# Kernel optimization log

Measured on AMD Instinct MI355X. Metric: run time of the kernel, lower is better.

The kernel has to match this reference:

```python
import jax, jax.numpy as jnp
import numpy as np

N = 8192
D_IN = 256
D_OUT = 256
DROP_P = 0.5


def setup_inputs() -> dict:
    key = jax.random.key(0)
    k1, k2, k3, k4, k5 = jax.random.split(key, 5)
    inputs = jax.random.normal(k1, (N, D_IN), dtype=jnp.float32)
    # torch nn.Linear weights are [d_out, d_in], applied as x @ W.T
    Wq = jax.random.normal(k2, (D_OUT, D_IN), dtype=jnp.float32) * (1.0 / np.sqrt(D_IN))
    Wk = jax.random.normal(k3, (D_OUT, D_IN), dtype=jnp.float32) * (1.0 / np.sqrt(D_IN))
    Wv = jax.random.normal(k4, (D_OUT, D_IN), dtype=jnp.float32) * (1.0 / np.sqrt(D_IN))
    # deterministic dropout keep-mask (True = keep), p=0.5
    drop_mask = jax.random.bernoulli(k5, 1.0 - DROP_P, (N, N))
    return {"inputs": inputs, "Wq": Wq, "Wk": Wk, "Wv": Wv, "drop_mask": drop_mask}


def reference(inputs, Wq, Wk, Wv, drop_mask):
    # QKV projections (no bias)
    q = inputs @ Wq.T  # [N, d_out]
    k = inputs @ Wk.T  # [N, d_out]
    v = inputs @ Wv.T  # [N, d_out]

    d_k = k.shape[1]
    scores = q @ k.T  # [N, N]

    # causal mask: strictly-upper-triangular entries -> -inf
    n = scores.shape[0]
    causal = jnp.triu(jnp.ones((n, n), dtype=bool), k=1)
    masked = jnp.where(causal, -jnp.inf, scores)

    attn_weights = jax.nn.softmax(masked / jnp.sqrt(jnp.float32(d_k)), axis=-1)

    # dropout p=0.5 in train mode: zero dropped entries, scale kept by 1/(1-p)
    scale = jnp.float32(1.0 / (1.0 - DROP_P))
    attn_weights = jnp.where(drop_mask, attn_weights * scale, 0.0)

    context_vector = attn_weights @ v  # [N, d_out]
    return context_vector
```

## Files before the change

### kernel.cpp

```cpp
#include <hip/hip_runtime.h>

#define NT 8192
#define DM 256

typedef float f32x16 __attribute__((ext_vector_type(16)));
typedef float f32x4 __attribute__((ext_vector_type(4)));
typedef __bf16 bf16x8 __attribute__((ext_vector_type(8)));
typedef unsigned int u32x4 __attribute__((ext_vector_type(4)));

#define MFMA32(a, b, c) __builtin_amdgcn_mfma_f32_32x32x16_bf16((a), (b), (c), 0, 0, 0)
#define MFMA16(a, b, c) __builtin_amdgcn_mfma_f32_16x16x32_bf16((a), (b), (c), 0, 0, 0)
#define NEG_INF (-__builtin_inff())

static __device__ __forceinline__ unsigned short f2bf_bits(float f) {
  return __builtin_bit_cast(unsigned short, (__bf16)f);
}
static __device__ __forceinline__ float exp2_fast(float x) {
  return __builtin_amdgcn_exp2f(x);
}
static __device__ __forceinline__ void gload_lds16(const void* g, void* l) {
  __builtin_amdgcn_global_load_lds(
      (const __attribute__((address_space(1))) unsigned int*)g,
      (__attribute__((address_space(3))) unsigned int*)l, 16, 0, 0);
}

__global__ __launch_bounds__(256) void maskpack_kernel(
    const void* __restrict__ mask, unsigned long long* __restrict__ bm) {
  const int t = threadIdx.x, lane = t & 63, w = t >> 6;
  const int r = blockIdx.x + (w << 11);
  const unsigned int* md = (const unsigned int*)mask;
  bool a01 = true, af = true;
#pragma unroll
  for (int k = 0; k < 4; ++k) {
    unsigned int v = md[lane + 64 * k];
    a01 = a01 && (v <= 1u);
    af = af && (v == 0u || v == 0x3F800000u);
  }
  const bool dword_mode = __all(a01) || __all(af);
  unsigned long long* out = bm + (size_t)r * 128;
  if (dword_mode) {
    const unsigned int* mk = (const unsigned int*)mask + (size_t)r * NT;
    const int iters = (r >> 8) + 1;
    for (int it = 0; it < iters; ++it) {
      const int j0 = it * 256;
      unsigned int v0 = mk[j0 + lane];
      unsigned int v1 = mk[j0 + 64 + lane];
      unsigned int v2 = mk[j0 + 128 + lane];
      unsigned int v3 = mk[j0 + 192 + lane];
      unsigned long long b0 = __ballot(v0 != 0u);
      unsigned long long b1 = __ballot(v1 != 0u);
      unsigned long long b2 = __ballot(v2 != 0u);
      unsigned long long b3 = __ballot(v3 != 0u);
      if (lane == 0) {
        out[(j0 >> 6) + 0] = b0;
        out[(j0 >> 6) + 1] = b1;
        out[(j0 >> 6) + 2] = b2;
        out[(j0 >> 6) + 3] = b3;
      }
    }
  } else {
    const unsigned char* mk = (const unsigned char*)mask + (size_t)r * NT;
    unsigned short* outs = (unsigned short*)out;
    const int iters = (r >> 10) + 1;
    for (int it = 0; it < iters; ++it) {
      const uint4 d = *(const uint4*)(mk + it * 1024 + lane * 16);
      unsigned int dws[4] = {d.x, d.y, d.z, d.w};
      unsigned int m16 = 0;
#pragma unroll
      for (int k = 0; k < 4; ++k) {
        unsigned int x = dws[k];
        x |= x >> 4;
        x |= x >> 2;
        x |= x >> 1;
        x &= 0x01010101u;
        m16 |= ((x * 0x01020408u) >> 24) << (4 * k);
      }
      outs[it * 64 + lane] = (unsigned short)m16;
    }
  }
}

__global__ __launch_bounds__(256) void proj_kernel(
    const float* __restrict__ X, const float* __restrict__ Wq,
    const float* __restrict__ Wk, const float* __restrict__ Wv,
    unsigned short* __restrict__ Qs, unsigned short* __restrict__ Kb,
    unsigned short* __restrict__ Vt) {
  __shared__ __align__(16) unsigned short Xs[64 * 256];
  __shared__ __align__(16) unsigned short Ws[64 * 256];
  __shared__ float Tr[4][32 * 33];
  const int ib = blockIdx.x, mat = blockIdx.y;
  const float* W = (mat == 0) ? Wq : (mat == 1) ? Wk : Wv;
  const float wscale = (mat == 0) ? 0.09016844005556021f : (mat == 2 ? 2.0f : 1.0f);
  const int t = threadIdx.x;
  const int lane = t & 63, w = t >> 6;
  const int m = lane & 31, half = lane >> 5;
  const int i0 = ib * 64;
#pragma unroll
  for (int cc = 0; cc < 8; ++cc) {
    int chunk = t + 256 * cc;
    int rr = chunk >> 5, c = chunk & 31;
    const float4* src = (const float4*)(X + (size_t)(i0 + rr) * 256 + c * 8);
    float4 f0 = src[0], f1 = src[1];
    bf16x8 v;
    v[0] = (__bf16)f0.x; v[1] = (__bf16)f0.y; v[2] = (__bf16)f0.z; v[3] = (__bf16)f0.w;
    v[4] = (__bf16)f1.x; v[5] = (__bf16)f1.y; v[6] = (__bf16)f1.z; v[7] = (__bf16)f1.w;
    *(bf16x8*)&Xs[(rr * 32 + (c ^ (rr & 31))) * 8] = v;
  }
  const int wr = w >> 1, wc = w & 1;
  for (int cb = 0; cb < 4; ++cb) {
    __syncthreads();
#pragma unroll
    for (int cc = 0; cc < 8; ++cc) {
      int chunk = t + 256 * cc;
      int rr = chunk >> 5, c = chunk & 31;
      const float4* src = (const float4*)(W + (size_t)(cb * 64 + rr) * 256 + c * 8);
      float4 f0 = src[0], f1 = src[1];
      bf16x8 v;
      v[0] = (__bf16)(f0.x * wscale); v[1] = (__bf16)(f0.y * wscale);
      v[2] = (__bf16)(f0.z * wscale); v[3] = (__bf16)(f0.w * wscale);
      v[4] = (__bf16)(f1.x * wscale); v[5] = (__bf16)(f1.y * wscale);
      v[6] = (__bf16)(f1.z * wscale); v[7] = (__bf16)(f1.w * wscale);
      *(bf16x8*)&Ws[(rr * 32 + (c ^ (rr & 31))) * 8] = v;
    }
    __syncthreads();
    f32x16 acc = {};
    const int ar = 32 * wr + m;
    const int br = 32 * wc + m;
#pragma unroll
    for (int st = 0; st < 16; ++st) {
      int kc = st * 2 + half;
      bf16x8 a = *(const bf16x8*)&Xs[(ar * 32 + (kc ^ (ar & 31))) * 8];
      bf16x8 b = *(const bf16x8*)&Ws[(br * 32 + (kc ^ (br & 31))) * 8];
      acc = MFMA32(a, b, acc);
    }
    if (mat < 2) {
      unsigned short* O = mat ? Kb : Qs;
#pragma unroll
      for (int r = 0; r < 16; ++r) {
        int row = i0 + 32 * wr + (r & 3) + 8 * (r >> 2) + 4 * half;
        int col = cb * 64 + 32 * wc + m;
        O[(size_t)row * DM + col] = f2bf_bits(acc[r]);
      }
    } else {
      float* T = Tr[w];
#pragma unroll
      for (int r = 0; r < 16; ++r) {
        int rl = (r & 3) + 8 * (r >> 2) + 4 * half;
        T[m * 33 + rl] = acc[r];
      }
      asm volatile("s_waitcnt lgkmcnt(0)" ::: "memory");
#pragma unroll
      for (int q = 0; q < 16; ++q) {
        int dl = 2 * q + half;
        float val = T[dl * 33 + m];
        Vt[(size_t)(cb * 64 + 32 * wc + dl) * NT + i0 + 32 * wr + m] = f2bf_bits(val);
      }
      asm volatile("s_waitcnt lgkmcnt(0)" ::: "memory");
    }
  }
}

__global__ __launch_bounds__(256, 3) void flash_kernel(
    const unsigned short* __restrict__ Qs, const unsigned short* __restrict__ Kg,
    const unsigned short* __restrict__ Vtg, const unsigned int* __restrict__ bm,
    float* __restrict__ ml_out, unsigned short* __restrict__ acc_out) {
  __shared__ __align__(16) unsigned short Ksh[32 * 256];
  __shared__ __align__(16) unsigned short Vsh[256 * 32];
  const int ib = blockIdx.x;
  const int seg = blockIdx.y;
  const int jb_end = 2 * (ib + 1);
  const int jb0 = seg * 16;
  if (jb0 >= jb_end) return;
  const int jb1 = (jb0 + 16 < jb_end) ? jb0 + 16 : jb_end;
  const int t = threadIdx.x, lane = t & 63, w = t >> 6;
  const int m = lane & 15, q = lane >> 4;
  const int i0 = ib * 64, rw0 = i0 + 16 * w;
  const int myrow = rw0 + m;

  bf16x8 qf[8];
  {
    const unsigned short* qp = Qs + (size_t)myrow * DM + q * 8;
#pragma unroll
    for (int st = 0; st < 8; ++st) qf[st] = *(const bf16x8*)(qp + st * 32);
  }
  f32x4 oacc[16] = {};
  float mrun = -1e30f, lrun = 0.f;

#define STAGE(JB)                                                             \
  {                                                                           \
    const int j32_ = (JB) * 32;                                               \
    _Pragma("unroll") for (int i_ = 0; i_ < 4; ++i_) {                        \
      int chunk = t + 256 * i_;                                               \
      int row = chunk >> 5, slot = chunk & 31;                                \
      gload_lds16(Kg + (size_t)(j32_ + row) * DM + (slot ^ row) * 8,          \
                  Ksh + (size_t)chunk * 8);                                   \
    }                                                                         \
    _Pragma("unroll") for (int i_ = 0; i_ < 4; ++i_) {                        \
      int chunk = t + 256 * i_;                                               \
      int d_ = chunk >> 2, slot = chunk & 3;                                  \
      gload_lds16(Vtg + (size_t)d_ * NT + j32_ + (slot ^ (d_ & 3)) * 8,       \
                  Vsh + (size_t)chunk * 8);                                   \
    }                                                                         \
  }

  STAGE(jb0)
  unsigned int bits = bm[(size_t)myrow * 256 + jb0];
  for (int jb = jb0; jb < jb1; ++jb) {
    const int j32 = jb * 32;
    __syncthreads();
    if (j32 <= rw0 + 15) {
      f32x4 s[2] = {};
#pragma unroll
      for (int st = 0; st < 8; ++st) {
        int kc = st * 4 + q;
#pragma unroll
        for (int ct = 0; ct < 2; ++ct) {
          int jr = ct * 16 + m;
          bf16x8 a = *(const bf16x8*)&Ksh[(jr * 32 + (kc ^ jr)) * 8];
          s[ct] = MFMA16(a, qf[st], s[ct]);
        }
      }
      if (j32 + 31 > rw0) {
#pragma unroll
        for (int ct = 0; ct < 2; ++ct)
#pragma unroll
          for (int r = 0; r < 4; ++r)
            if (j32 + ct * 16 + q * 4 + r > myrow) s[ct][r] = NEG_INF;
      }
      float mx = fmaxf(fmaxf(fmaxf(s[0][0], s[0][1]), fmaxf(s[0][2], s[0][3])),
                       fmaxf(fmaxf(s[1][0], s[1][1]), fmaxf(s[1][2], s[1][3])));
      mx = fmaxf(mx, __shfl_xor(mx, 16));
      mx = fmaxf(mx, __shfl_xor(mx, 32));
      const float mn = fmaxf(mrun, mx);
#pragma unroll
      for (int ct = 0; ct < 2; ++ct)
#pragma unroll
        for (int r = 0; r < 4; ++r) s[ct][r] = exp2_fast(s[ct][r] - mn);
      float rs = (s[0][0] + s[0][1]) + (s[0][2] + s[0][3]) +
                 (s[1][0] + s[1][1]) + (s[1][2] + s[1][3]);
      rs += __shfl_xor(rs, 16);
      rs += __shfl_xor(rs, 32);
      if (__all(mn == mrun)) {
        lrun += rs;
      } else {
        float alpha = exp2_fast(mrun - mn);
        lrun = lrun * alpha + rs;
#pragma unroll
        for (int ct = 0; ct < 16; ++ct)
#pragma unroll
          for (int r = 0; r < 4; ++r) oacc[ct][r] *= alpha;
        mrun = mn;
      }
      unsigned int A0, A1, B0, B1;
      {
        unsigned int bbA = bits >> (q * 4);
        unsigned int bbB = bits >> (16 + q * 4);
        float a0 = (bbA & 1u) ? s[0][0] : 0.f, a1 = (bbA & 2u) ? s[0][1] : 0.f;
        float a2 = (bbA & 4u) ? s[0][2] : 0.f, a3 = (bbA & 8u) ? s[0][3] : 0.f;
        float b0 = (bbB & 1u) ? s[1][0] : 0.f, b1 = (bbB & 2u) ? s[1][1] : 0.f;
        float b2 = (bbB & 4u) ? s[1][2] : 0.f, b3 = (bbB & 8u) ? s[1][3] : 0.f;
        A0 = (unsigned)f2bf_bits(a0) | ((unsigned)f2bf_bits(a1) << 16);
        A1 = (unsigned)f2bf_bits(a2) | ((unsigned)f2bf_bits(a3) << 16);
        B0 = (unsigned)f2bf_bits(b0) | ((unsigned)f2bf_bits(b1) << 16);
        B1 = (unsigned)f2bf_bits(b2) | ((unsigned)f2bf_bits(b3) << 16);
      }
      unsigned int own0 = (q & 2) ? B0 : A0, own1 = (q & 2) ? B1 : A1;
      unsigned int sA0 = (q & 2) ? A0 : B0, sA1 = (q & 2) ? A1 : B1;
      unsigned int r10 = __shfl_xor(sA0, 32);
      unsigned int r11 = __shfl_xor(sA1, 32);
      const bool selOwn = ((q ^ (q >> 1)) & 1) != 0;
      unsigned int s20 = selOwn ? own0 : r10;
      unsigned int s21 = selOwn ? own1 : r11;
      unsigned int r20 = __shfl_xor(s20, 16);
      unsigned int r21 = __shfl_xor(s21, 16);
      unsigned int lo0 = (q == 0) ? A0 : (q == 2) ? r10 : r20;
      unsigned int lo1 = (q == 0) ? A1 : (q == 2) ? r11 : r21;
      unsigned int hi0 = (q == 3) ? B0 : (q == 1) ? r10 : r20;
      unsigned int hi1 = (q == 3) ? B1 : (q == 1) ? r11 : r21;
      bf16x8 pf = __builtin_bit_cast(bf16x8, (u32x4){lo0, lo1, hi0, hi1});
#pragma unroll
      for (int ct = 0; ct < 16; ++ct) {
        int d = ct * 16 + m;
        bf16x8 a = *(const bf16x8*)&Vsh[(d * 4 + (q ^ (d & 3))) * 8];
        oacc[ct] = MFMA16(a, pf, oacc[ct]);
      }
    }
    __syncthreads();
    if (jb + 1 < jb1) {
      STAGE(jb + 1)
      bits = bm[(size_t)myrow * 256 + jb + 1];
    }
  }
#undef STAGE
  const int a_ = ib >> 3, r_ = ib & 7;
  const int g = 4 * a_ * (a_ + 1) + r_ * (a_ + 1) + seg;
  if (q == 0) {
    float* mlb = ml_out + ((size_t)g * 64 + 16 * w + m) * 2;
    mlb[0] = mrun;
    mlb[1] = lrun;
  }
  unsigned short* ab = acc_out + ((size_t)g * 64 + 16 * w + m) * DM;
#pragma unroll
  for (int ct = 0; ct < 16; ++ct) {
    unsigned long long pk = 0;
#pragma unroll
    for (int r = 0; r < 4; ++r)
      pk |= (unsigned long long)f2bf_bits(oacc[ct][r]) << (16 * r);
    *(unsigned long long*)&ab[ct * 16 + q * 4] = pk;
  }
}

__global__ __launch_bounds__(256) void combine_kernel(
    const float* __restrict__ ml, const unsigned short* __restrict__ pacc,
    float* __restrict__ out) {
  const int t = threadIdx.x;
  const int row = blockIdx.x * 32 + (t >> 3);
  const int cg = (t & 7) * 32;
  const int ib = row >> 6, rib = row & 63;
  const int a = ib >> 3, r = ib & 7;
  const int g0 = 4 * a * (a + 1) + r * (a + 1);
  const int ns = a + 1;
  float M = -1e30f;
  for (int s = 0; s < ns; ++s) M = fmaxf(M, ml[((size_t)(g0 + s) * 64 + rib) * 2]);
  float Wd = 0.f;
  float acc[32];
#pragma unroll
  for (int j = 0; j < 32; ++j) acc[j] = 0.f;
  for (int s = 0; s < ns; ++s) {
    const float* mls = ml + ((size_t)(g0 + s) * 64 + rib) * 2;
    float wv = exp2_fast(mls[0] - M);
    Wd += wv * mls[1];
    const unsigned short* pa = pacc + ((size_t)(g0 + s) * 64 + rib) * DM + cg;
#pragma unroll
    for (int v4 = 0; v4 < 4; ++v4) {
      bf16x8 b = *(const bf16x8*)(pa + v4 * 8);
#pragma unroll
      for (int j = 0; j < 8; ++j) acc[v4 * 8 + j] += wv * (float)b[j];
    }
  }
  float inv = 1.0f / Wd;
#pragma unroll
  for (int j = 0; j < 32; ++j) out[(size_t)row * DM + cg + j] = acc[j] * inv;
}

extern "C" void kernel_launch(void* const* d_in, const int* in_sizes, int n_in,
                              void* d_out, int out_size, void* d_ws, size_t ws_size,
                              hipStream_t stream) {
  const float* X  = (const float*)d_in[0];
  const float* Wq = (const float*)d_in[1];
  const float* Wk = (const float*)d_in[2];
  const float* Wv = (const float*)d_in[3];
  const void* mask = d_in[4];
  float* out = (float*)d_out;

  char* ws = (char*)d_ws;
  unsigned short* Qs = (unsigned short*)(ws + 4096);
  unsigned short* Kb = Qs + (size_t)NT * DM;
  unsigned short* Vt = Kb + (size_t)NT * DM;
  float* ml = (float*)(Vt + (size_t)NT * DM);
  unsigned short* pacc = (unsigned short*)(ml + (size_t)1088 * 64 * 2);
  unsigned long long* bmw = (unsigned long long*)((char*)pacc + (size_t)1088 * 64 * DM * 2);

  maskpack_kernel<<<2048, 256, 0, stream>>>(mask, bmw);
  proj_kernel<<<dim3(128, 3), 256, 0, stream>>>(X, Wq, Wk, Wv, Qs, Kb, Vt);
  flash_kernel<<<dim3(128, 16), 256, 0, stream>>>(Qs, Kb, Vt, (const unsigned int*)bmw,
                                                  ml, pacc);
  combine_kernel<<<256, 256, 0, stream>>>(ml, pacc, out);
}
```

Baseline: 467.5 us.

## Double flash kernel key tile from 32 to 64 columns per iteration

The flash attention kernel now handles 64 key/value columns per loop iteration instead of 32. K and V shared-memory tiles grow to 64 columns, the mask is read as 64-bit words, and the P fragment is built as two butterfly-packed halves feeding two MFMAs per output tile. This halves the number of syncthreads, softmax max/sum reductions and rescale checks per key, at the cost of twice the LDS per block and launch bounds lowered from 3 to 2 blocks per CU. Segment bookkeeping is scaled to match, keeping 8 tiles of 64 per segment.

```diff
diff --git a/kernel.cpp b/kernel.cpp
--- a/kernel.cpp
+++ b/kernel.cpp
@@ -160,18 +160,49 @@
   }
 }
 
-__global__ __launch_bounds__(256, 3) void flash_kernel(
+static __device__ __forceinline__ bf16x8 pack_butterfly(const f32x4 sA, const f32x4 sB,
+                                                        unsigned int bits, int q) {
+  unsigned int A0, A1, B0, B1;
+  {
+    unsigned int bbA = bits >> (q * 4);
+    unsigned int bbB = bits >> (16 + q * 4);
+    float a0 = (bbA & 1u) ? sA[0] : 0.f, a1 = (bbA & 2u) ? sA[1] : 0.f;
+    float a2 = (bbA & 4u) ? sA[2] : 0.f, a3 = (bbA & 8u) ? sA[3] : 0.f;
+    float b0 = (bbB & 1u) ? sB[0] : 0.f, b1 = (bbB & 2u) ? sB[1] : 0.f;
+    float b2 = (bbB & 4u) ? sB[2] : 0.f, b3 = (bbB & 8u) ? sB[3] : 0.f;
+    A0 = (unsigned)f2bf_bits(a0) | ((unsigned)f2bf_bits(a1) << 16);
+    A1 = (unsigned)f2bf_bits(a2) | ((unsigned)f2bf_bits(a3) << 16);
+    B0 = (unsigned)f2bf_bits(b0) | ((unsigned)f2bf_bits(b1) << 16);
+    B1 = (unsigned)f2bf_bits(b2) | ((unsigned)f2bf_bits(b3) << 16);
+  }
+  unsigned int own0 = (q & 2) ? B0 : A0, own1 = (q & 2) ? B1 : A1;
+  unsigned int t0 = (q & 2) ? A0 : B0, t1 = (q & 2) ? A1 : B1;
+  unsigned int r10 = __shfl_xor(t0, 32);
+  unsigned int r11 = __shfl_xor(t1, 32);
+  const bool selOwn = ((q ^ (q >> 1)) & 1) != 0;
+  unsigned int s20 = selOwn ? own0 : r10;
+  unsigned int s21 = selOwn ? own1 : r11;
+  unsigned int r20 = __shfl_xor(s20, 16);
+  unsigned int r21 = __shfl_xor(s21, 16);
+  unsigned int lo0 = (q == 0) ? A0 : (q == 2) ? r10 : r20;
+  unsigned int lo1 = (q == 0) ? A1 : (q == 2) ? r11 : r21;
+  unsigned int hi0 = (q == 3) ? B0 : (q == 1) ? r10 : r20;
+  unsigned int hi1 = (q == 3) ? B1 : (q == 1) ? r11 : r21;
+  return __builtin_bit_cast(bf16x8, (u32x4){lo0, lo1, hi0, hi1});
+}
+
+__global__ __launch_bounds__(256, 2) void flash_kernel(
     const unsigned short* __restrict__ Qs, const unsigned short* __restrict__ Kg,
-    const unsigned short* __restrict__ Vtg, const unsigned int* __restrict__ bm,
+    const unsigned short* __restrict__ Vtg, const unsigned long long* __restrict__ bm,
     float* __restrict__ ml_out, unsigned short* __restrict__ acc_out) {
-  __shared__ __align__(16) unsigned short Ksh[32 * 256];
-  __shared__ __align__(16) unsigned short Vsh[256 * 32];
+  __shared__ __align__(16) unsigned short Ksh[64 * 256];
+  __shared__ __align__(16) unsigned short Vsh[256 * 64];
   const int ib = blockIdx.x;
   const int seg = blockIdx.y;
-  const int jb_end = 2 * (ib + 1);
-  const int jb0 = seg * 16;
+  const int jb_end = ib + 1;
+  const int jb0 = seg * 8;
   if (jb0 >= jb_end) return;
-  const int jb1 = (jb0 + 16 < jb_end) ? jb0 + 16 : jb_end;
+  const int jb1 = (jb0 + 8 < jb_end) ? jb0 + 8 : jb_end;
   const int t = threadIdx.x, lane = t & 63, w = t >> 6;
   const int m = lane & 15, q = lane >> 4;
   const int i0 = ib * 64, rw0 = i0 + 16 * w;
@@ -188,56 +219,60 @@
 
 #define STAGE(JB)                                                             \
   {                                                                           \
-    const int j32_ = (JB) * 32;                                               \
-    _Pragma("unroll") for (int i_ = 0; i_ < 4; ++i_) {                        \
+    const int j64_ = (JB) * 64;                                               \
+    _Pragma("unroll") for (int i_ = 0; i_ < 8; ++i_) {                        \
       int chunk = t + 256 * i_;                                               \
       int row = chunk >> 5, slot = chunk & 31;                                \
-      gload_lds16(Kg + (size_t)(j32_ + row) * DM + (slot ^ row) * 8,          \
+      gload_lds16(Kg + (size_t)(j64_ + row) * DM + (slot ^ (row & 31)) * 8,   \
                   Ksh + (size_t)chunk * 8);                                   \
     }                                                                         \
-    _Pragma("unroll") for (int i_ = 0; i_ < 4; ++i_) {                        \
+    _Pragma("unroll") for (int i_ = 0; i_ < 8; ++i_) {                        \
       int chunk = t + 256 * i_;                                               \
-      int d_ = chunk >> 2, slot = chunk & 3;                                  \
-      gload_lds16(Vtg + (size_t)d_ * NT + j32_ + (slot ^ (d_ & 3)) * 8,       \
+      int d_ = chunk >> 3, slot = chunk & 7;                                  \
+      gload_lds16(Vtg + (size_t)d_ * NT + j64_ + (slot ^ (d_ & 7)) * 8,       \
                   Vsh + (size_t)chunk * 8);                                   \
     }                                                                         \
   }
 
   STAGE(jb0)
-  unsigned int bits = bm[(size_t)myrow * 256 + jb0];
+  unsigned long long bits = bm[(size_t)myrow * 128 + jb0];
   for (int jb = jb0; jb < jb1; ++jb) {
-    const int j32 = jb * 32;
+    const int j64 = jb * 64;
     __syncthreads();
-    if (j32 <= rw0 + 15) {
-      f32x4 s[2] = {};
+    if (j64 <= rw0 + 15) {
+      f32x4 s[4] = {};
 #pragma unroll
       for (int st = 0; st < 8; ++st) {
         int kc = st * 4 + q;
 #pragma unroll
-        for (int ct = 0; ct < 2; ++ct) {
+        for (int ct = 0; ct < 4; ++ct) {
           int jr = ct * 16 + m;
-          bf16x8 a = *(const bf16x8*)&Ksh[(jr * 32 + (kc ^ jr)) * 8];
+          bf16x8 a = *(const bf16x8*)&Ksh[(jr * 32 + (kc ^ (jr & 31))) * 8];
           s[ct] = MFMA16(a, qf[st], s[ct]);
         }
       }
-      if (j32 + 31 > rw0) {
-#pragma unroll
-        for (int ct = 0; ct < 2; ++ct)
+      if (j64 + 63 > rw0) {
+#pragma unroll
+        for (int ct = 0; ct < 4; ++ct)
 #pragma unroll
           for (int r = 0; r < 4; ++r)
-            if (j32 + ct * 16 + q * 4 + r > myrow) s[ct][r] = NEG_INF;
+            if (j64 + ct * 16 + q * 4 + r > myrow) s[ct][r] = NEG_INF;
       }
       float mx = fmaxf(fmaxf(fmaxf(s[0][0], s[0][1]), fmaxf(s[0][2], s[0][3])),
                        fmaxf(fmaxf(s[1][0], s[1][1]), fmaxf(s[1][2], s[1][3])));
+      mx = fmaxf(mx, fmaxf(fmaxf(fmaxf(s[2][0], s[2][1]), fmaxf(s[2][2], s[2][3])),
+                           fmaxf(fmaxf(s[3][0], s[3][1]), fmaxf(s[3][2], s[3][3]))));
       mx = fmaxf(mx, __shfl_xor(mx, 16));
       mx = fmaxf(mx, __shfl_xor(mx, 32));
       const float mn = fmaxf(mrun, mx);
 #pragma unroll
-      for (int ct = 0; ct < 2; ++ct)
+      for (int ct = 0; ct < 4; ++ct)
 #pragma unroll
         for (int r = 0; r < 4; ++r) s[ct][r] = exp2_fast(s[ct][r] - mn);
-      float rs = (s[0][0] + s[0][1]) + (s[0][2] + s[0][3]) +
-                 (s[1][0] + s[1][1]) + (s[1][2] + s[1][3]);
+      float rs = ((s[0][0] + s[0][1]) + (s[0][2] + s[0][3])) +
+                 ((s[1][0] + s[1][1]) + (s[1][2] + s[1][3])) +
+                 ((s[2][0] + s[2][1]) + (s[2][2] + s[2][3])) +
+                 ((s[3][0] + s[3][1]) + (s[3][2] + s[3][3]));
       rs += __shfl_xor(rs, 16);
       rs += __shfl_xor(rs, 32);
       if (__all(mn == mrun)) {
@@ -251,44 +286,21 @@
           for (int r = 0; r < 4; ++r) oacc[ct][r] *= alpha;
         mrun = mn;
       }
-      unsigned int A0, A1, B0, B1;
-      {
-        unsigned int bbA = bits >> (q * 4);
-        unsigned int bbB = bits >> (16 + q * 4);
-        float a0 = (bbA & 1u) ? s[0][0] : 0.f, a1 = (bbA & 2u) ? s[0][1] : 0.f;
-        float a2 = (bbA & 4u) ? s[0][2] : 0.f, a3 = (bbA & 8u) ? s[0][3] : 0.f;
-        float b0 = (bbB & 1u) ? s[1][0] : 0.f, b1 = (bbB & 2u) ? s[1][1] : 0.f;
-        float b2 = (bbB & 4u) ? s[1][2] : 0.f, b3 = (bbB & 8u) ? s[1][3] : 0.f;
-        A0 = (unsigned)f2bf_bits(a0) | ((unsigned)f2bf_bits(a1) << 16);
-        A1 = (unsigned)f2bf_bits(a2) | ((unsigned)f2bf_bits(a3) << 16);
-        B0 = (unsigned)f2bf_bits(b0) | ((unsigned)f2bf_bits(b1) << 16);
-        B1 = (unsigned)f2bf_bits(b2) | ((unsigned)f2bf_bits(b3) << 16);
-      }
-      unsigned int own0 = (q & 2) ? B0 : A0, own1 = (q & 2) ? B1 : A1;
-      unsigned int sA0 = (q & 2) ? A0 : B0, sA1 = (q & 2) ? A1 : B1;
-      unsigned int r10 = __shfl_xor(sA0, 32);
-      unsigned int r11 = __shfl_xor(sA1, 32);
-      const bool selOwn = ((q ^ (q >> 1)) & 1) != 0;
-      unsigned int s20 = selOwn ? own0 : r10;
-      unsigned int s21 = selOwn ? own1 : r11;
-      unsigned int r20 = __shfl_xor(s20, 16);
-      unsigned int r21 = __shfl_xor(s21, 16);
-      unsigned int lo0 = (q == 0) ? A0 : (q == 2) ? r10 : r20;
-      unsigned int lo1 = (q == 0) ? A1 : (q == 2) ? r11 : r21;
-      unsigned int hi0 = (q == 3) ? B0 : (q == 1) ? r10 : r20;
-      unsigned int hi1 = (q == 3) ? B1 : (q == 1) ? r11 : r21;
-      bf16x8 pf = __builtin_bit_cast(bf16x8, (u32x4){lo0, lo1, hi0, hi1});
+      bf16x8 pf0 = pack_butterfly(s[0], s[1], (unsigned int)bits, q);
+      bf16x8 pf1 = pack_butterfly(s[2], s[3], (unsigned int)(bits >> 32), q);
 #pragma unroll
       for (int ct = 0; ct < 16; ++ct) {
         int d = ct * 16 + m;
-        bf16x8 a = *(const bf16x8*)&Vsh[(d * 4 + (q ^ (d & 3))) * 8];
-        oacc[ct] = MFMA16(a, pf, oacc[ct]);
+        bf16x8 a0 = *(const bf16x8*)&Vsh[(d * 8 + (q ^ (d & 7))) * 8];
+        bf16x8 a1 = *(const bf16x8*)&Vsh[(d * 8 + ((q + 4) ^ (d & 7))) * 8];
+        oacc[ct] = MFMA16(a0, pf0, oacc[ct]);
+        oacc[ct] = MFMA16(a1, pf1, oacc[ct]);
       }
     }
     __syncthreads();
     if (jb + 1 < jb1) {
       STAGE(jb + 1)
-      bits = bm[(size_t)myrow * 256 + jb + 1];
+      bits = bm[(size_t)myrow * 128 + jb + 1];
     }
   }
 #undef STAGE
@@ -363,7 +375,6 @@
 
   maskpack_kernel<<<2048, 256, 0, stream>>>(mask, bmw);
   proj_kernel<<<dim3(128, 3), 256, 0, stream>>>(X, Wq, Wk, Wv, Qs, Kb, Vt);
-  flash_kernel<<<dim3(128, 16), 256, 0, stream>>>(Qs, Kb, Vt, (const unsigned int*)bmw,
-                                                  ml, pacc);
+  flash_kernel<<<dim3(128, 16), 256, 0, stream>>>(Qs, Kb, Vt, bmw, ml, pacc);
   combine_kernel<<<256, 256, 0, stream>>>(ml, pacc, out);
 }
```

Result: faster. 458.0 us (-2.0%).
